# Optimization experiments

Measured on AMD Instinct MI355X. Metric: run time of the kernel, lower is better.

The kernel has to match this reference:

```python
import jax, jax.numpy as jnp
import numpy as np

N_NODES = 50000
N_EDGES = 800000
IN_FEATS = 128
N_HIDDEN = 128
N_CLASSES = 16


def setup_inputs() -> dict:
    key = jax.random.key(0)
    ks = jax.random.split(key, 10)
    d = {
        'x': jax.random.normal(ks[0], (N_NODES, IN_FEATS), dtype=jnp.float32),
        'src': jax.random.randint(ks[1], (N_EDGES,), 0, N_NODES, dtype=jnp.int32),
        'dst': jax.random.randint(ks[2], (N_EDGES,), 0, N_NODES, dtype=jnp.int32),
    }
    sc = 1.0 / np.sqrt(N_HIDDEN)
    d['w_self0'] = jax.random.normal(ks[3], (IN_FEATS, N_HIDDEN), dtype=jnp.float32) * sc
    d['w_neigh0'] = jax.random.normal(ks[4], (IN_FEATS, N_HIDDEN), dtype=jnp.float32) * sc
    d['b0'] = jnp.zeros((N_HIDDEN,), dtype=jnp.float32)
    d['w_self1'] = jax.random.normal(ks[5], (N_HIDDEN, N_HIDDEN), dtype=jnp.float32) * sc
    d['w_neigh1'] = jax.random.normal(ks[6], (N_HIDDEN, N_HIDDEN), dtype=jnp.float32) * sc
    d['b1'] = jnp.zeros((N_HIDDEN,), dtype=jnp.float32)
    d['w_self2'] = jax.random.normal(ks[7], (N_HIDDEN, N_HIDDEN), dtype=jnp.float32) * sc
    d['w_neigh2'] = jax.random.normal(ks[8], (N_HIDDEN, N_HIDDEN), dtype=jnp.float32) * sc
    d['b2'] = jnp.zeros((N_HIDDEN,), dtype=jnp.float32)
    d['w_head'] = jax.random.normal(ks[9], (N_HIDDEN, N_CLASSES), dtype=jnp.float32) * sc
    d['b_head'] = jnp.zeros((N_CLASSES,), dtype=jnp.float32)
    return d


def _sage_conv(h, src, dst, inv_deg, w_self, w_neigh, b):
    # mean aggregator: gather src features, scatter-add to dst, divide by in-degree
    agg = jax.ops.segment_sum(h[src], dst, num_segments=N_NODES)  # [N, d]
    neigh = agg * inv_deg[:, None]
    return h @ w_self + neigh @ w_neigh + b


def reference(x, src, dst, w_self0, w_neigh0, b0, w_self1, w_neigh1, b1,
              w_self2, w_neigh2, b2, w_head, b_head):
    deg = jax.ops.segment_sum(jnp.ones((src.shape[0],), jnp.float32), dst,
                              num_segments=N_NODES)
    inv_deg = 1.0 / jnp.maximum(deg, 1.0)
    h = x  # dropout is identity in eval mode
    for (ws, wn, b) in ((w_self0, w_neigh0, b0),
                        (w_self1, w_neigh1, b1),
                        (w_self2, w_neigh2, b2)):
        h = jax.nn.relu(_sage_conv(h, src, dst, inv_deg, ws, wn, b))
    pls = jnp.mean(h, axis=0, keepdims=True)  # AvgPooling over single graph -> [1, n_hidden]
    score = pls @ w_head + b_head  # [1, n_classes]
    return (score, pls)
```

## Files before the change

kernel.cpp:

```cpp
#include <hip/hip_runtime.h>
#include <hip/hip_bf16.h>
#include <hip/hip_fp8.h>
#include <stdint.h>

#define NN 50000
#define NE 800000
#define F 128
#define NCLS 16
#define NB 196
#define BCAP 5120
#define PA_EPT 16
#define PW_BLKS 192
#define CV_BLKS 6250

typedef __attribute__((ext_vector_type(8))) short short8;
typedef __attribute__((ext_vector_type(4))) float f32x4;
typedef __attribute__((ext_vector_type(2))) float f32x2;
typedef __attribute__((ext_vector_type(4))) unsigned int uint4v;

#define OB_COLSUM    0u
#define OB_BCUR      512u
#define OB_ROWSTART  4096u
#define OB_INVDEG    204800u
#define OB_PAIRS     409600u
#define OB_SRCS16    4423680u
#define OB_WT        6023680u
#define OB_XB        6220800u
#define OB_HB1       19020800u
#define OB_X8        31820800u
#define OB_F8A       38220800u
#define OB_NB        44620800u

__device__ __forceinline__ uint32_t swz_off(uint32_t row, uint32_t k) {
    uint32_t c = ((k >> 5) << 2) | ((k >> 2) & 3u);
    uint32_t b = (((k >> 4) & 1u) << 3) | ((k & 3u) << 1);
    return (row << 8) + (((c ^ (row & 15u)) << 4) | b);
}

__device__ __forceinline__ uint32_t pack_bf2(float a, float b) {
    __hip_bfloat16 l = __float2bfloat16(a), h = __float2bfloat16(b);
    return ((uint32_t)(*(uint16_t*)&h) << 16) | (uint32_t)(*(uint16_t*)&l);
}

__device__ __forceinline__ uint8_t f32_to_fp8(float v) {
#if __has_builtin(__builtin_amdgcn_cvt_pk_fp8_f32)
    return (uint8_t)(__builtin_amdgcn_cvt_pk_fp8_f32(v, 0.f, 0, false) & 0xff);
#else
    __hip_fp8_e4m3 t(v);
    return t.__x;
#endif
}

__device__ __forceinline__ uint32_t f32x4_to_fp8x4(float a, float b, float c, float d) {
#if __has_builtin(__builtin_amdgcn_cvt_pk_fp8_f32)
    int r = __builtin_amdgcn_cvt_pk_fp8_f32(a, b, 0, false);
    r = __builtin_amdgcn_cvt_pk_fp8_f32(c, d, r, true);
    return (uint32_t)r;
#else
    __hip_fp8_e4m3 ta(a), tb(b), tc(c), td(d);
    return (uint32_t)ta.__x | ((uint32_t)tb.__x << 8) | ((uint32_t)tc.__x << 16) | ((uint32_t)td.__x << 24);
#endif
}

__device__ __forceinline__ void acc4(uint32_t d, f32x2& p0, f32x2& p1) {
#if __has_builtin(__builtin_amdgcn_cvt_pk_f32_fp8)
    p0 += __builtin_amdgcn_cvt_pk_f32_fp8((int)d, false);
    p1 += __builtin_amdgcn_cvt_pk_f32_fp8((int)d, true);
#else
    __hip_fp8_e4m3 t0, t1, t2, t3;
    t0.__x = (uint8_t)(d & 0xff); t1.__x = (uint8_t)((d >> 8) & 0xff);
    t2.__x = (uint8_t)((d >> 16) & 0xff); t3.__x = (uint8_t)((d >> 24) & 0xff);
    p0.x += (float)t0; p0.y += (float)t1; p1.x += (float)t2; p1.y += (float)t3;
#endif
}

__device__ __forceinline__ void gload16(const void* g, void* l) {
    __builtin_amdgcn_global_load_lds(
        (const __attribute__((address_space(1))) unsigned int*)g,
        (__attribute__((address_space(3))) unsigned int*)l, 16, 0, 0);
}

__global__ __launch_bounds__(256) void fused_prep(
        const float* __restrict__ x, uint8_t* __restrict__ xb, uint8_t* __restrict__ x8,
        const float* __restrict__ w0, const float* __restrict__ w1,
        const float* __restrict__ w2, const float* __restrict__ w3,
        const float* __restrict__ w4, const float* __restrict__ w5,
        uint8_t* __restrict__ wt,
        const int* __restrict__ src, const int* __restrict__ dst,
        int* __restrict__ bcur, uint32_t* __restrict__ pairs) {
    __shared__ int cnt[NB];
    __shared__ int base_s[NB];
    int bid = blockIdx.x;
    int t = threadIdx.x;

    if (bid < NB) {
        for (int i = t; i < NB; i += 256) cnt[i] = 0;
        __syncthreads();
        uint32_t pk[PA_EPT];
        int bk[PA_EPT];
        int e0 = bid * (256 * PA_EPT) + t;
#pragma unroll
        for (int j = 0; j < PA_EPT; ++j) {
            int e = e0 + j * 256;
            if (e < NE) {
                int sv = src[e], dv = dst[e];
                bk[j] = dv >> 8;
                pk[j] = (uint32_t)sv | (((uint32_t)dv & 255u) << 16);
                atomicAdd(&cnt[bk[j]], 1);
            } else bk[j] = -1;
        }
        __syncthreads();
        for (int i = t; i < NB; i += 256) {
            if (cnt[i] > 0) base_s[i] = i * BCAP + atomicAdd(&bcur[i], cnt[i]);
            cnt[i] = 0;
        }
        __syncthreads();
#pragma unroll
        for (int j = 0; j < PA_EPT; ++j) {
            if (bk[j] >= 0) {
                int pos = base_s[bk[j]] + atomicAdd(&cnt[bk[j]], 1);
                pairs[pos] = pk[j];
            }
        }
        return;
    }
    bid -= NB;
    if (bid < PW_BLKS) {
        int m = bid >> 5;
        const float* w = m == 0 ? w0 : m == 1 ? w1 : m == 2 ? w2 : m == 3 ? w3 : m == 4 ? w4 : w5;
        int tt = (bid & 31) * 256 + t;
        int n = tt >> 6;
        int k0 = (tt & 63) << 1;
        uint32_t pk = pack_bf2(w[k0 * F + n], w[(k0 + 1) * F + n]);
        *(uint32_t*)(wt + (uint32_t)m * 32768u + swz_off((uint32_t)n, (uint32_t)k0)) = pk;
        return;
    }
    bid -= PW_BLKS;
    int tt = bid * 256 + t;
    uint32_t row = (uint32_t)tt >> 5;
    uint32_t q = (uint32_t)tt & 31u;
    float4 v = *(const float4*)(x + row * F + q * 4);
    uint32_t c = ((q >> 3) << 2) | (q & 3u);
    uint32_t hi = (q >> 2) & 1u;
    uint2 pk;
    pk.x = pack_bf2(v.x, v.y);
    pk.y = pack_bf2(v.z, v.w);
    *(uint2*)(xb + (row << 8) + (((c ^ (row & 15u)) << 4) | (hi << 3))) = pk;
    *(uint32_t*)(x8 + row * 128u + q * 4u) = f32x4_to_fp8x4(v.x, v.y, v.z, v.w);
}

__global__ __launch_bounds__(256) void pass_b(const uint32_t* __restrict__ pairs,
                                              const int* __restrict__ bcur,
                                              int* __restrict__ row_start,
                                              float* __restrict__ inv_deg,
                                              unsigned short* __restrict__ srcs) {
    __shared__ int sarr[256];
    __shared__ int cnt[256];
    __shared__ int cur[256];
    int b = blockIdx.x, t = threadIdx.x;
    sarr[t] = (t < NB) ? bcur[t] : 0;
    __syncthreads();
    for (int off = 1; off < 256; off <<= 1) {
        int u = (t >= off) ? sarr[t - off] : 0;
        __syncthreads();
        sarr[t] += u;
        __syncthreads();
    }
    int fill = bcur[b];
    int out0 = sarr[b] - fill;
    int in0 = b * BCAP;
    cnt[t] = 0;
    __syncthreads();
    for (int i = t; i < fill; i += 256)
        atomicAdd(&cnt[pairs[in0 + i] >> 16], 1);
    __syncthreads();
    int v = cnt[t];
    sarr[t] = v;
    __syncthreads();
    for (int off = 1; off < 256; off <<= 1) {
        int u = (t >= off) ? sarr[t - off] : 0;
        __syncthreads();
        sarr[t] += u;
        __syncthreads();
    }
    int excl = sarr[t] - v;
    cur[t] = out0 + excl;
    int row = (b << 8) + t;
    if (row < NN) {
        row_start[row] = out0 + excl;
        inv_deg[row] = 1.0f / (float)(v > 1 ? v : 1);
    }
    if (b == 0 && t == 0) row_start[NN] = NE;
    __syncthreads();
    for (int i = t; i < fill; i += 256) {
        uint32_t p = pairs[in0 + i];
        int pos = atomicAdd(&cur[p >> 16], 1);
        srcs[pos] = (unsigned short)(p & 0xffffu);
    }
}

__global__ __launch_bounds__(256) void aggregate_f8(
        const uint8_t* __restrict__ hf8, const int* __restrict__ row_start,
        const unsigned short* __restrict__ srcs, const float* __restrict__ inv_deg,
        uint8_t* __restrict__ nb) {
    int node = blockIdx.x * 4 + (threadIdx.x >> 6);
    int l = threadIdx.x & 63;
    int g = l >> 3;
    uint32_t m = (uint32_t)(l & 7);
    const uint8_t* base = hf8 + m * 16u;
    int e0 = row_start[node], e1 = row_start[node + 1];
    f32x2 a[8];
#pragma unroll
    for (int i = 0; i < 8; ++i) { a[i].x = 0.f; a[i].y = 0.f; }

    int e = e0;
    for (; e + 16 <= e1; e += 16) {
        uint32_t sa = srcs[e + g];
        uint32_t sb = srcs[e + 8 + g];
        uint4 da = *(const uint4*)(base + ((uint32_t)sa << 7));
        uint4 db = *(const uint4*)(base + ((uint32_t)sb << 7));
        acc4(da.x, a[0], a[1]); acc4(da.y, a[2], a[3]);
        acc4(da.z, a[4], a[5]); acc4(da.w, a[6], a[7]);
        acc4(db.x, a[0], a[1]); acc4(db.y, a[2], a[3]);
        acc4(db.z, a[4], a[5]); acc4(db.w, a[6], a[7]);
    }
    if (e + 8 <= e1) {
        uint32_t sa = srcs[e + g];
        uint4 da = *(const uint4*)(base + ((uint32_t)sa << 7));
        acc4(da.x, a[0], a[1]); acc4(da.y, a[2], a[3]);
        acc4(da.z, a[4], a[5]); acc4(da.w, a[6], a[7]);
        e += 8;
    }
    if (e + g < e1) {
        uint32_t sa = srcs[e + g];
        uint4 da = *(const uint4*)(base + ((uint32_t)sa << 7));
        acc4(da.x, a[0], a[1]); acc4(da.y, a[2], a[3]);
        acc4(da.z, a[4], a[5]); acc4(da.w, a[6], a[7]);
    }
#pragma unroll
    for (int d = 8; d < 64; d <<= 1) {
#pragma unroll
        for (int i = 0; i < 8; ++i) {
            a[i].x += __shfl_xor(a[i].x, d);
            a[i].y += __shfl_xor(a[i].y, d);
        }
    }
    if (g == 0) {
        float idg = inv_deg[node];
        uint32_t rx = (uint32_t)node & 15u;
        char* rowp = (char*)nb + ((uint32_t)node << 8);
        uint32_t bh = (m & 1u) << 3;
#pragma unroll
        for (int jj = 0; jj < 4; ++jj) {
            uint32_t c = ((m >> 1) << 2) | (uint32_t)jj;
            uint2 w;
            w.x = pack_bf2(a[2 * jj].x * idg, a[2 * jj].y * idg);
            w.y = pack_bf2(a[2 * jj + 1].x * idg, a[2 * jj + 1].y * idg);
            *(uint2*)(rowp + (((c ^ rx) << 4) | bh)) = w;
        }
    }
}

__global__ __launch_bounds__(256) void gemm_mfma(
        const uint8_t* __restrict__ a_self, const uint8_t* __restrict__ a_neigh,
        const uint8_t* __restrict__ wt_self, const uint8_t* __restrict__ wt_neigh,
        const float* __restrict__ bias, uint8_t* __restrict__ hout,
        uint8_t* hout_f8, float* colsum) {
    __shared__ uint4v As4[1024];
    __shared__ uint4v Ws4[2048];
    __shared__ float cs[128];
    int tid = threadIdx.x;
    int lane = tid & 63, wave = tid >> 6;
    int rl = lane & 15, g = lane >> 4;
    int row0 = blockIdx.x * 64;

    f32x4 acc[8];
    f32x4 z = {0.f, 0.f, 0.f, 0.f};
#pragma unroll
    for (int nt = 0; nt < 8; ++nt) acc[nt] = z;

    const char* AsB = (const char*)As4;
    const char* WsB = (const char*)Ws4;

#pragma unroll
    for (int pass = 0; pass < 2; ++pass) {
        if (pass) __syncthreads();
        const uint4v* ga = (const uint4v*)((pass ? a_neigh : a_self) + (size_t)row0 * 256);
        const uint4v* gw = (const uint4v*)(pass ? wt_neigh : wt_self);
#pragma unroll
        for (int i = 0; i < 4; ++i) gload16(&ga[tid + i * 256], &As4[tid + i * 256]);
#pragma unroll
        for (int i = 0; i < 8; ++i) gload16(&gw[tid + i * 256], &Ws4[tid + i * 256]);
        __syncthreads();
#pragma unroll
        for (int ks = 0; ks < 4; ++ks) {
            int chunk = ((ks << 2) | g) ^ rl;
            short8 a = *(const short8*)(AsB + ((wave * 16 + rl) << 8) + (chunk << 4));
#pragma unroll
            for (int nt = 0; nt < 8; ++nt) {
                short8 bb = *(const short8*)(WsB + ((nt * 16 + rl) << 8) + (chunk << 4));
                acc[nt] = __builtin_amdgcn_mfma_f32_16x16x32_bf16(a, bb, acc[nt], 0, 0, 0);
            }
        }
    }

    bool doCol = (colsum != nullptr);
    bool doF8 = (hout_f8 != nullptr);
    if (doCol) {
        if (tid < 128) cs[tid] = 0.f;
        __syncthreads();
    }
#pragma unroll
    for (int nt = 0; nt < 8; ++nt) {
        int col = nt * 16 + rl;
        float bv = bias[col];
        float rsum = 0.f;
#pragma unroll
        for (int i = 0; i < 4; ++i) {
            int row = row0 + wave * 16 + g * 4 + i;
            if (row < NN) {
                float v = fmaxf(acc[nt][i] + bv, 0.f);
                rsum += v;
                *(__hip_bfloat16*)(hout + swz_off((uint32_t)row, (uint32_t)col)) =
                    __float2bfloat16(v);
                if (doF8) hout_f8[(uint32_t)row * 128u + (uint32_t)col] = f32_to_fp8(v);
            }
        }
        if (doCol) atomicAdd(&cs[col], rsum);
    }
    if (doCol) {
        __syncthreads();
        if (tid < 128) atomicAdd(&colsum[tid], cs[tid]);
    }
}

__global__ __launch_bounds__(128) void head_kernel(const float* __restrict__ colsum,
                                                   const float* __restrict__ w_head,
                                                   const float* __restrict__ b_head,
                                                   float* __restrict__ out) {
    __shared__ float pls[F];
    int t = threadIdx.x;
    float p = colsum[t] * (1.0f / (float)NN);
    pls[t] = p;
    out[NCLS + t] = p;
    __syncthreads();
    if (t < NCLS) {
        float sc = b_head[t];
        for (int f = 0; f < F; ++f) sc += pls[f] * w_head[f * NCLS + t];
        out[t] = sc;
    }
}

extern "C" void kernel_launch(void* const* d_in, const int* in_sizes, int n_in,
                              void* d_out, int out_size, void* d_ws, size_t ws_size,
                              hipStream_t stream) {
    const float* x       = (const float*)d_in[0];
    const int*   src     = (const int*)d_in[1];
    const int*   dst     = (const int*)d_in[2];
    const float* w_self0 = (const float*)d_in[3];
    const float* w_neigh0= (const float*)d_in[4];
    const float* b0      = (const float*)d_in[5];
    const float* w_self1 = (const float*)d_in[6];
    const float* w_neigh1= (const float*)d_in[7];
    const float* b1      = (const float*)d_in[8];
    const float* w_self2 = (const float*)d_in[9];
    const float* w_neigh2= (const float*)d_in[10];
    const float* b2      = (const float*)d_in[11];
    const float* w_head  = (const float*)d_in[12];
    const float* b_head  = (const float*)d_in[13];
    float* out = (float*)d_out;

    uint8_t* ws = (uint8_t*)d_ws;
    float* colsum   = (float*)(ws + OB_COLSUM);
    int*   bcur     = (int*)(ws + OB_BCUR);
    int*   row_start= (int*)(ws + OB_ROWSTART);
    float* inv_deg  = (float*)(ws + OB_INVDEG);
    uint32_t* pairs = (uint32_t*)(ws + OB_PAIRS);
    unsigned short* srcs16 = (unsigned short*)(ws + OB_SRCS16);
    uint8_t* wt     = ws + OB_WT;
    uint8_t* xb     = ws + OB_XB;
    uint8_t* hb1    = ws + OB_HB1;
    uint8_t* x8     = ws + OB_X8;
    uint8_t* f8a    = ws + OB_F8A;
    uint8_t* nb     = ws + OB_NB;

    hipMemsetAsync(d_ws, 0, 1536, stream);

    fused_prep<<<NB + PW_BLKS + CV_BLKS, 256, 0, stream>>>(
        x, xb, x8, w_self0, w_neigh0, w_self1, w_neigh1, w_self2, w_neigh2, wt,
        src, dst, bcur, pairs);
    pass_b<<<NB, 256, 0, stream>>>(pairs, bcur, row_start, inv_deg, srcs16);

    const int GB = (NN + 63) / 64;

    aggregate_f8<<<12500, 256, 0, stream>>>(x8, row_start, srcs16, inv_deg, nb);
    gemm_mfma<<<GB, 256, 0, stream>>>(xb, nb, wt + 0 * 32768, wt + 1 * 32768, b0,
                                      hb1, f8a, nullptr);
    aggregate_f8<<<12500, 256, 0, stream>>>(f8a, row_start, srcs16, inv_deg, nb);
    gemm_mfma<<<GB, 256, 0, stream>>>(hb1, nb, wt + 2 * 32768, wt + 3 * 32768, b1,
                                      xb, x8, nullptr);
    aggregate_f8<<<12500, 256, 0, stream>>>(x8, row_start, srcs16, inv_deg, nb);
    gemm_mfma<<<GB, 256, 0, stream>>>(xb, nb, wt + 4 * 32768, wt + 5 * 32768, b2,
                                      hb1, nullptr, colsum);

    head_kernel<<<1, 128, 0, stream>>>(colsum, w_head, b_head, out);
}
```

Baseline: 204.3 us.

## Unroll aggregate gather to 32 edges and double GEMM row tile to 128

The aggregation loop now issues four independent 16-byte gathers per iteration instead of two, which puts more loads in flight to hide gather latency, and the leftover edges are handled by a loop over groups of 8. The GEMM block now covers 128 rows instead of 64: each wave computes two 16-row tiles, so every weight tile loaded into LDS is reused twice as often and half as many blocks are launched. This raises register and LDS use per block (A tile doubled), which can lower occupancy. Grid size becomes about 391 blocks, fewer than twice the CU count, so some CUs may sit idle.

After: 186.7 us. 1.09x faster.

```diff
diff --git a/kernel.cpp b/kernel.cpp
--- a/kernel.cpp
+++ b/kernel.cpp
@@ -214,26 +214,33 @@
     for (int i = 0; i < 8; ++i) { a[i].x = 0.f; a[i].y = 0.f; }
 
     int e = e0;
-    for (; e + 16 <= e1; e += 16) {
+    for (; e + 32 <= e1; e += 32) {
+        uint32_t s0 = srcs[e + g];
+        uint32_t s1 = srcs[e + 8 + g];
+        uint32_t s2 = srcs[e + 16 + g];
+        uint32_t s3 = srcs[e + 24 + g];
+        uint4 d0 = *(const uint4*)(base + (s0 << 7));
+        uint4 d1 = *(const uint4*)(base + (s1 << 7));
+        uint4 d2 = *(const uint4*)(base + (s2 << 7));
+        uint4 d3 = *(const uint4*)(base + (s3 << 7));
+        acc4(d0.x, a[0], a[1]); acc4(d0.y, a[2], a[3]);
+        acc4(d0.z, a[4], a[5]); acc4(d0.w, a[6], a[7]);
+        acc4(d1.x, a[0], a[1]); acc4(d1.y, a[2], a[3]);
+        acc4(d1.z, a[4], a[5]); acc4(d1.w, a[6], a[7]);
+        acc4(d2.x, a[0], a[1]); acc4(d2.y, a[2], a[3]);
+        acc4(d2.z, a[4], a[5]); acc4(d2.w, a[6], a[7]);
+        acc4(d3.x, a[0], a[1]); acc4(d3.y, a[2], a[3]);
+        acc4(d3.z, a[4], a[5]); acc4(d3.w, a[6], a[7]);
+    }
+    for (; e + 8 <= e1; e += 8) {
         uint32_t sa = srcs[e + g];
-        uint32_t sb = srcs[e + 8 + g];
-        uint4 da = *(const uint4*)(base + ((uint32_t)sa << 7));
-        uint4 db = *(const uint4*)(base + ((uint32_t)sb << 7));
+        uint4 da = *(const uint4*)(base + (sa << 7));
         acc4(da.x, a[0], a[1]); acc4(da.y, a[2], a[3]);
         acc4(da.z, a[4], a[5]); acc4(da.w, a[6], a[7]);
-        acc4(db.x, a[0], a[1]); acc4(db.y, a[2], a[3]);
-        acc4(db.z, a[4], a[5]); acc4(db.w, a[6], a[7]);
-    }
-    if (e + 8 <= e1) {
-        uint32_t sa = srcs[e + g];
-        uint4 da = *(const uint4*)(base + ((uint32_t)sa << 7));
-        acc4(da.x, a[0], a[1]); acc4(da.y, a[2], a[3]);
-        acc4(da.z, a[4], a[5]); acc4(da.w, a[6], a[7]);
-        e += 8;
     }
     if (e + g < e1) {
         uint32_t sa = srcs[e + g];
-        uint4 da = *(const uint4*)(base + ((uint32_t)sa << 7));
+        uint4 da = *(const uint4*)(base + (sa << 7));
         acc4(da.x, a[0], a[1]); acc4(da.y, a[2], a[3]);
         acc4(da.z, a[4], a[5]); acc4(da.w, a[6], a[7]);
     }
@@ -266,18 +273,20 @@
         const uint8_t* __restrict__ wt_self, const uint8_t* __restrict__ wt_neigh,
         const float* __restrict__ bias, uint8_t* __restrict__ hout,
         uint8_t* hout_f8, float* colsum) {
-    __shared__ uint4v As4[1024];
+    __shared__ uint4v As4[2048];
     __shared__ uint4v Ws4[2048];
     __shared__ float cs[128];
     int tid = threadIdx.x;
     int lane = tid & 63, wave = tid >> 6;
     int rl = lane & 15, g = lane >> 4;
-    int row0 = blockIdx.x * 64;
-
-    f32x4 acc[8];
+    int row0 = blockIdx.x * 128;
+
+    f32x4 acc[2][8];
     f32x4 z = {0.f, 0.f, 0.f, 0.f};
 #pragma unroll
-    for (int nt = 0; nt < 8; ++nt) acc[nt] = z;
+    for (int rt = 0; rt < 2; ++rt)
+#pragma unroll
+        for (int nt = 0; nt < 8; ++nt) acc[rt][nt] = z;
 
     const char* AsB = (const char*)As4;
     const char* WsB = (const char*)Ws4;
@@ -288,18 +297,21 @@
         const uint4v* ga = (const uint4v*)((pass ? a_neigh : a_self) + (size_t)row0 * 256);
         const uint4v* gw = (const uint4v*)(pass ? wt_neigh : wt_self);
 #pragma unroll
-        for (int i = 0; i < 4; ++i) gload16(&ga[tid + i * 256], &As4[tid + i * 256]);
+        for (int i = 0; i < 8; ++i) gload16(&ga[tid + i * 256], &As4[tid + i * 256]);
 #pragma unroll
         for (int i = 0; i < 8; ++i) gload16(&gw[tid + i * 256], &Ws4[tid + i * 256]);
         __syncthreads();
 #pragma unroll
         for (int ks = 0; ks < 4; ++ks) {
             int chunk = ((ks << 2) | g) ^ rl;
-            short8 a = *(const short8*)(AsB + ((wave * 16 + rl) << 8) + (chunk << 4));
-#pragma unroll
-            for (int nt = 0; nt < 8; ++nt) {
-                short8 bb = *(const short8*)(WsB + ((nt * 16 + rl) << 8) + (chunk << 4));
-                acc[nt] = __builtin_amdgcn_mfma_f32_16x16x32_bf16(a, bb, acc[nt], 0, 0, 0);
+#pragma unroll
+            for (int rt = 0; rt < 2; ++rt) {
+                short8 a = *(const short8*)(AsB + ((wave * 32 + rt * 16 + rl) << 8) + (chunk << 4));
+#pragma unroll
+                for (int nt = 0; nt < 8; ++nt) {
+                    short8 bb = *(const short8*)(WsB + ((nt * 16 + rl) << 8) + (chunk << 4));
+                    acc[rt][nt] = __builtin_amdgcn_mfma_f32_16x16x32_bf16(a, bb, acc[rt][nt], 0, 0, 0);
+                }
             }
         }
     }
@@ -311,22 +323,25 @@
         __syncthreads();
     }
 #pragma unroll
-    for (int nt = 0; nt < 8; ++nt) {
-        int col = nt * 16 + rl;
-        float bv = bias[col];
-        float rsum = 0.f;
-#pragma unroll
-        for (int i = 0; i < 4; ++i) {
-            int row = row0 + wave * 16 + g * 4 + i;
-            if (row < NN) {
-                float v = fmaxf(acc[nt][i] + bv, 0.f);
-                rsum += v;
-                *(__hip_bfloat16*)(hout + swz_off((uint32_t)row, (uint32_t)col)) =
-                    __float2bfloat16(v);
-                if (doF8) hout_f8[(uint32_t)row * 128u + (uint32_t)col] = f32_to_fp8(v);
+    for (int rt = 0; rt < 2; ++rt) {
+#pragma unroll
+        for (int nt = 0; nt < 8; ++nt) {
+            int col = nt * 16 + rl;
+            float bv = bias[col];
+            float rsum = 0.f;
+#pragma unroll
+            for (int i = 0; i < 4; ++i) {
+                int row = row0 + wave * 32 + rt * 16 + g * 4 + i;
+                if (row < NN) {
+                    float v = fmaxf(acc[rt][nt][i] + bv, 0.f);
+                    rsum += v;
+                    *(__hip_bfloat16*)(hout + swz_off((uint32_t)row, (uint32_t)col)) =
+                        __float2bfloat16(v);
+                    if (doF8) hout_f8[(uint32_t)row * 128u + (uint32_t)col] = f32_to_fp8(v);
+                }
             }
-        }
-        if (doCol) atomicAdd(&cs[col], rsum);
+            if (doCol) atomicAdd(&cs[col], rsum);
+        }
     }
     if (doCol) {
         __syncthreads();
@@ -391,7 +406,7 @@
         src, dst, bcur, pairs);
     pass_b<<<NB, 256, 0, stream>>>(pairs, bcur, row_start, inv_deg, srcs16);
 
-    const int GB = (NN + 63) / 64;
+    const int GB = (NN + 127) / 128;
 
     aggregate_f8<<<12500, 256, 0, stream>>>(x8, row_start, srcs16, inv_deg, nb);
     gemm_mfma<<<GB, 256, 0, stream>>>(xb, nb, wt + 0 * 32768, wt + 1 * 32768, b0,
```
